# Optimization experiments

Measured on AMD Instinct MI355X. Metric: run time of the kernel, lower is better.

Reference implementation:

```python
import jax, jax.numpy as jnp
import numpy as np

EPS = 1e-10
BETA = 1.0  # beta passed to VectorQuantizer in Encoder_conv


def _conv(x, w, b, stride, pad):
    # x: NCHW, w: OIHW
    y = jax.lax.conv_general_dilated(x, w, window_strides=stride, padding=pad,
                                     dimension_numbers=('NCHW', 'OIHW', 'NCHW'))
    if b is not None:
        y = y + b[None, :, None, None]
    return y


def _forward(x, w_in, b_in, w_h1, b_h1, w_h2, b_h2, w_h3, b_h3,
             r0_w1, r0_w2, r1_w1, r1_w2, emb):
    relu = jax.nn.relu
    h = relu(_conv(x, w_in, b_in, (2, 2), [(1, 1), (1, 1)]))      # [B,128,256,256]
    h = relu(_conv(h, w_h1, b_h1, (4, 4), [(2, 2), (2, 2)]))      # [B,256,64,64]
    h = relu(_conv(h, w_h2, b_h2, (4, 4), [(2, 2), (2, 2)]))      # [B,256,16,16]
    h = relu(_conv(h, w_h3, b_h3, (2, 2), [(1, 1), (1, 1)]))      # [B,256,8,8]
    # ResidualBlock with 2 Residual layers: relu->conv[1,3]->relu->conv[1,1], no bias
    for wa, wb in ((r0_w1, r0_w2), (r1_w1, r1_w2)):
        t = _conv(relu(h), wa, None, (1, 1), [(0, 0), (1, 1)])
        t = _conv(relu(t), wb, None, (1, 1), [(0, 0), (0, 0)])
        h = h + t
    h = relu(h)
    # VectorQuantizer
    lat = jnp.transpose(h, (0, 2, 3, 1))                          # [B,H,W,D]
    D = emb.shape[1]
    flat = lat.reshape(-1, D)                                     # [N,D]
    dist = (jnp.sum(flat * flat, axis=1, keepdims=True)
            + jnp.sum(emb * emb, axis=1)
            - 2.0 * flat @ emb.T)                                 # [N,K]
    idx = jnp.argmin(dist, axis=1)                                # [N]
    quant = emb[idx].reshape(lat.shape)                           # [B,H,W,D]
    sg = jax.lax.stop_gradient
    e_loss = jnp.mean((sg(quant) - lat) ** 2)
    q_loss = jnp.mean((quant - sg(lat)) ** 2)
    loss = q_loss + BETA * e_loss
    quant_st = lat + sg(quant - lat)                              # straight-through
    probs = jnp.mean(jax.nn.one_hot(idx, emb.shape[0], dtype=lat.dtype), axis=0)
    perplexity = jnp.exp(-jnp.sum(probs * jnp.log(probs + EPS)))
    return jnp.transpose(quant_st, (0, 3, 1, 2)), loss, perplexity


def setup_inputs() -> dict:
    key = jax.random.key(0)
    ks = jax.random.split(key, 14)
    C_in, C, K = 3, 256, 512
    s = 0.05
    f32 = jnp.float32
    return {
        'x':     jax.random.normal(ks[0], (8, C_in, 512, 512), f32),
        'w_in':  jax.random.normal(ks[1], (C // 2, C_in, 4, 4), f32) * s,
        'b_in':  jnp.zeros((C // 2,), f32),
        'w_h1':  jax.random.normal(ks[2], (C, C // 2, 7, 7), f32) * s,
        'b_h1':  jnp.zeros((C,), f32),
        'w_h2':  jax.random.normal(ks[3], (C, C, 7, 7), f32) * s,
        'b_h2':  jnp.zeros((C,), f32),
        'w_h3':  jax.random.normal(ks[4], (C, C, 3, 3), f32) * s,
        'b_h3':  jnp.zeros((C,), f32),
        'r0_w1': jax.random.normal(ks[5], (4 * C, C, 1, 3), f32) * s,
        'r0_w2': jax.random.normal(ks[6], (C, 4 * C, 1, 1), f32) * s,
        'r1_w1': jax.random.normal(ks[7], (4 * C, C, 1, 3), f32) * s,
        'r1_w2': jax.random.normal(ks[8], (C, 4 * C, 1, 1), f32) * s,
        'emb':   jax.random.uniform(ks[9], (K, C), f32, -1.0 / K, 1.0 / K),
    }


def reference(x, w_in, b_in, w_h1, b_h1, w_h2, b_h2, w_h3, b_h3,
              r0_w1, r0_w2, r1_w1, r1_w2, emb):
    return _forward(x, w_in, b_in, w_h1, b_h1, w_h2, b_h2, w_h3, b_h3,
                    r0_w1, r0_w2, r1_w1, r1_w2, emb)
```

## Files before the change

### kernel.cpp

```cpp
#include <hip/hip_runtime.h>
#include <hip/hip_bf16.h>

typedef __hip_bfloat16 bf16;
typedef __attribute__((ext_vector_type(4))) float f32x4;
typedef __attribute__((ext_vector_type(8))) short short8;

__device__ __forceinline__ float b2f(bf16 v) { return __bfloat162float(v); }
__device__ __forceinline__ float bu2f(ushort u)
{
    union { uint i; float f; } c; c.i = (uint)u << 16; return c.f;
}
__device__ __forceinline__ ushort f2bu(float v)
{
    bf16 b = __float2bfloat16(v);
    return *(ushort*)&b;
}
__device__ __forceinline__ uint relu2(uint v)
{
    uint r = v;
    if (r & 0x8000u)     r &= 0xFFFF0000u;
    if (r & 0x80000000u) r &= 0x0000FFFFu;
    return r;
}
__device__ __forceinline__ uint packbf2(float a, float b)
{
    uint lo = f2bu(a), hi = f2bu(b);
    return lo | (hi << 16);
}

typedef const __attribute__((address_space(1))) unsigned int* as1_u32;
typedef __attribute__((address_space(3))) unsigned int* as3_u32;
__device__ __forceinline__ void gld16(const void* g, uint* l)
{
    __builtin_amdgcn_global_load_lds((as1_u32)g, (as3_u32)l, 16, 0, 0);
}

__global__ void init_k(const float* __restrict__ w_in, const float* __restrict__ w_h1,
        const float* __restrict__ w_h2, const float* __restrict__ w_h3,
        const float* __restrict__ r0w1, const float* __restrict__ r0w2,
        const float* __restrict__ r1w1, const float* __restrict__ r1w2,
        const float* __restrict__ emb,
        bf16* __restrict__ wp1, bf16* __restrict__ wpack2, bf16* __restrict__ wpack3,
        bf16* __restrict__ wp4, bf16* __restrict__ wpA0, bf16* __restrict__ wpA1,
        bf16* __restrict__ wpB0, bf16* __restrict__ wpB1,
        float* __restrict__ en, float* __restrict__ mse, int* __restrict__ hist,
        float* __restrict__ zpad, float* __restrict__ p3)
{
    long long i = (long long)blockIdx.x * 256 + threadIdx.x;
    if (i < 8192) {
        int j = i & 7; int co = (i >> 3) & 127; int kb = i >> 10;
        int k = kb * 8 + j;
        wp1[i] = __float2bfloat16(k < 48 ? w_in[co * 48 + k] : 0.f);
        return;
    }
    i -= 8192;
    if (i < 1638400) {
        int cil = i & 7; int co = (i >> 3) & 255; int r = i >> 11;
        int cib8 = r % 16; int tap = r / 16;
        float v = (tap < 49) ? w_h1[(size_t)co * 6272 + (cib8 * 8 + cil) * 49 + tap] : 0.f;
        wpack2[i] = __float2bfloat16(v);
        return;
    }
    i -= 1638400;
    if (i < 3276800) {
        int cil = i & 7; int co = (i >> 3) & 255; int r = i >> 11;
        int cib8 = r % 32; int tap = r / 32;
        float v = (tap < 49) ? w_h2[(size_t)co * 12544 + (cib8 * 8 + cil) * 49 + tap] : 0.f;
        wpack3[i] = __float2bfloat16(v);
        return;
    }
    i -= 3276800;
    if (i < 589824) {
        int cil = i & 7; int co = (i >> 3) & 255; int r = i >> 11;
        int cib8 = r % 32; int tap = r / 32;
        wp4[i] = __float2bfloat16(w_h3[(size_t)co * 2304 + (cib8 * 8 + cil) * 9 + tap]);
        return;
    }
    i -= 589824;
    if (i < 786432) {
        int cil = i & 7; int co = (i >> 3) & 1023; int r = i >> 13;
        int cib8 = r % 32; int tap = r / 32;
        wpA0[i] = __float2bfloat16(r0w1[(size_t)co * 768 + (cib8 * 8 + cil) * 3 + tap]);
        return;
    }
    i -= 786432;
    if (i < 786432) {
        int cil = i & 7; int co = (i >> 3) & 1023; int r = i >> 13;
        int cib8 = r % 32; int tap = r / 32;
        wpA1[i] = __float2bfloat16(r1w1[(size_t)co * 768 + (cib8 * 8 + cil) * 3 + tap]);
        return;
    }
    i -= 786432;
    if (i < 262144) {
        int cil = i & 7; int co = (i >> 3) & 255; int cib8 = (i >> 11) % 128;
        wpB0[i] = __float2bfloat16(r0w2[(size_t)co * 1024 + cib8 * 8 + cil]);
        return;
    }
    i -= 262144;
    if (i < 262144) {
        int cil = i & 7; int co = (i >> 3) & 255; int cib8 = (i >> 11) % 128;
        wpB1[i] = __float2bfloat16(r1w2[(size_t)co * 1024 + cib8 * 8 + cil]);
        return;
    }
    i -= 262144;
    if (i < 512) {
        const float* e = emb + (size_t)i * 256;
        float s = 0.f;
        for (int d = 0; d < 256; ++d) { float v = e[d]; s += v * v; }
        en[i] = s;
        return;
    }
    i -= 512;
    if (i < 577) {
        if (i == 0) mse[0] = 0.f;
        else if (i < 513) hist[i - 1] = 0;
        else zpad[i - 513] = 0.f;
        return;
    }
    i -= 577;
    if (i < 524288) p3[i] = 0.f;
}

__global__ __launch_bounds__(256) void conv1m_k(const float* __restrict__ x,
        const bf16* __restrict__ wp1, const float* __restrict__ bias,
        bf16* __restrict__ h1c)
{
    int bid = blockIdx.x;
    int pxt = bid & 511, img = bid >> 9;
    int tr = pxt >> 4, tc = pxt & 15;
    int oh0 = tr * 8, ow0 = tc * 16;
    const float* xi = x + (size_t)img * 786432;
    bf16* oT = h1c + (size_t)img * 8388608;

    int t = threadIdx.x;
    int wave = t >> 6, lane = t & 63;
    int quad = lane >> 4, l15 = lane & 15;

    __shared__ ushort xs[4 * 640];
    __shared__ ushort ot[128 * 136];

    int ihb = oh0 * 2 - 1, iwb = ow0 * 2 - 1;
    for (int i = t; i < 1836; i += 256) {
        int ci = i / 612; int r1 = i - ci * 612;
        int ihl = r1 / 34, iwl = r1 - ihl * 34;
        int ih = ihb + ihl, iw = iwb + iwl;
        float v = 0.f;
        if ((unsigned)ih < 512u && (unsigned)iw < 512u)
            v = xi[ci * 262144 + ih * 512 + iw];
        xs[ci * 640 + ihl * 35 + iwl] = f2bu(v);
    }
    for (int i = t; i < 640; i += 256) xs[3 * 640 + i] = 0;
    __syncthreads();

    f32x4 zero = {0.f, 0.f, 0.f, 0.f};
    f32x4 acc[8][2];
    #pragma unroll
    for (int m = 0; m < 8; ++m) { acc[m][0] = zero; acc[m][1] = zero; }

    int ci_b = quad >> 1;
    int kh0 = (quad & 1) * 2;
    int iwl0 = 2 * l15;

    #pragma unroll
    for (int ks = 0; ks < 2; ++ks) {
        union { short8 v; uint u[4]; } b[2];
        #pragma unroll
        for (int nt = 0; nt < 2; ++nt) {
            int py = wave * 2 + nt;
            int base = (ks * 2 + ci_b) * 640 + (2 * py + kh0) * 35 + iwl0;
            b[nt].u[0] = *(const uint*)&xs[base];
            b[nt].u[1] = *(const uint*)&xs[base + 2];
            b[nt].u[2] = *(const uint*)&xs[base + 35];
            b[nt].u[3] = *(const uint*)&xs[base + 37];
        }
        const bf16* abase = wp1 + ((size_t)(ks * 4 + quad) * 128 + l15) * 8;
        #pragma unroll
        for (int m = 0; m < 8; ++m) {
            short8 a = *(const short8*)(abase + m * 16 * 8);
            acc[m][0] = __builtin_amdgcn_mfma_f32_16x16x32_bf16(a, b[0].v, acc[m][0], 0, 0, 0);
            acc[m][1] = __builtin_amdgcn_mfma_f32_16x16x32_bf16(a, b[1].v, acc[m][1], 0, 0, 0);
        }
    }

    #pragma unroll
    for (int m = 0; m < 8; ++m) {
        int cobase = m * 16 + quad * 4;
        float b0 = bias[cobase], b1 = bias[cobase + 1];
        float b2 = bias[cobase + 2], b3 = bias[cobase + 3];
        #pragma unroll
        for (int nt = 0; nt < 2; ++nt) {
            int pxl = (wave * 2 + nt) * 16 + l15;
            uint w0 = packbf2(fmaxf(b0 + acc[m][nt][0], 0.f),
                              fmaxf(b1 + acc[m][nt][1], 0.f));
            uint w1 = packbf2(fmaxf(b2 + acc[m][nt][2], 0.f),
                              fmaxf(b3 + acc[m][nt][3], 0.f));
            *(uint*)&ot[pxl * 136 + cobase]     = w0;
            *(uint*)&ot[pxl * 136 + cobase + 2] = w1;
        }
    }
    __syncthreads();
    {
        int pxl = t >> 1, half = t & 1;
        int oh = oh0 + (pxl >> 4), ow = ow0 + (pxl & 15);
        size_t px = (size_t)(oh * 256 + ow);
        #pragma unroll
        for (int cb = 0; cb < 4; ++cb) {
            int c16 = half * 4 + cb;
            const uint4* src = (const uint4*)&ot[pxl * 136 + c16 * 16];
            uint4* dst = (uint4*)(oT + ((size_t)c16 * 65536 + px) * 16);
            dst[0] = src[0];
            dst[1] = src[1];
        }
    }
}

template <int IH, int OH, int CI, int SPLIT, int MODE>
__global__ __launch_bounds__(256) void conv_mfma6_k(
        const bf16* __restrict__ inC, const bf16* __restrict__ wpack,
        const float* __restrict__ bias, float* __restrict__ outA,
        bf16* __restrict__ outT, const float* __restrict__ zpad)
{
    constexpr int TPD = OH / 8;
    constexpr int NT = TPD * TPD;
    constexpr int CPB = (CI / 16) / SPLIT;
    constexpr int CIB8 = CI / 8;
    constexpr int NPX = IH * IH;
    constexpr int SLOTS = 2496;

    int bid = blockIdx.x;
    int pxt = bid % NT;
    int rest = bid / NT;
    int img = rest & 7;
    int split = rest >> 3;
    int oh0 = (pxt / TPD) * 8, ow0 = (pxt % TPD) * 8;

    int t = threadIdx.x;
    int wave = t >> 6, lane = t & 63;
    int quad = lane >> 4, l15 = lane & 15;

    const bf16* inb = inC + (size_t)img * ((size_t)NPX * CI);

    __shared__ __align__(16) uint bufA[SLOTS * 4];
    __shared__ __align__(16) uint bufB[SLOTS * 4];

    f32x4 zero = {0.f, 0.f, 0.f, 0.f};
    f32x4 acc[4][4];
    #pragma unroll
    for (int a = 0; a < 4; ++a)
        #pragma unroll
        for (int b = 0; b < 4; ++b) acc[a][b] = zero;

    int ihb = oh0 * 4 - 2, iwb = ow0 * 4 - 2;
    int qxl = l15 & 7, pyl = l15 >> 3;
    int tap_par = quad >> 1, ci_half = quad & 1;

    auto stage = [&](int ch, uint* dst) {
        const bf16* cb = inb + (size_t)ch * NPX * 16;
        auto issue = [&](int sb) {
            int p  = sb + lane;
            int pb = p << 4;
            int lb = pb ^ (((pb >> 7) & 7) << 4);
            int j  = lb >> 4;
            int pos = j >> 1, half = j & 1;
            int r = pos / 35, c = pos - r * 35;
            int ih = ihb + r, iw = iwb + c;
            const void* src = (const void*)zpad;
            if (j < 2450 && (unsigned)ih < (unsigned)IH && (unsigned)iw < (unsigned)IH)
                src = (const void*)(cb + ((size_t)ih * IH + iw) * 16 + half * 8);
            gld16(src, dst + sb * 4);
        };
        #pragma unroll
        for (int it = 0; it < 9; ++it) issue(it * 256 + wave * 64);
        if (wave < 3) issue(2304 + wave * 64);
    };

    auto compute = [&](int ch, const uint* cbuf) {
        const bf16* abase = wpack +
            ((size_t)(ch * 2 + ci_half) * 256 + wave * 64 + l15) * 8;
        for (int tp = 0; tp < 25; ++tp) {
            int tap = 2 * tp + tap_par;
            short8 a[4];
            #pragma unroll
            for (int ct = 0; ct < 4; ++ct)
                a[ct] = *(const short8*)(abase +
                    ((size_t)tap * CIB8 * 256 + ct * 16) * 8);
            int tapc = min(tap, 48);
            int kh = tapc / 7, kw = tapc - kh * 7;
            int p0 = (kh + 4 * pyl) * 35 + qxl * 4 + kw;
            #pragma unroll
            for (int pt = 0; pt < 4; ++pt) {
                int lb = ((p0 + pt * 280) * 2 + ci_half) << 4;
                int pb = lb ^ (((lb >> 7) & 7) << 4);
                short8 b = *(const short8*)((const char*)cbuf + pb);
                #pragma unroll
                for (int ct = 0; ct < 4; ++ct)
                    acc[ct][pt] = __builtin_amdgcn_mfma_f32_16x16x32_bf16(
                        a[ct], b, acc[ct][pt], 0, 0, 0);
            }
        }
    };

    stage(split * CPB, bufA);
    __syncthreads();
    for (int cc2 = 0; cc2 < CPB; cc2 += 2) {
        stage(split * CPB + cc2 + 1, bufB);
        compute(split * CPB + cc2, bufA);
        __syncthreads();
        if (cc2 + 2 < CPB) stage(split * CPB + cc2 + 2, bufA);
        compute(split * CPB + cc2 + 1, bufB);
        __syncthreads();
    }

    #pragma unroll
    for (int ct = 0; ct < 4; ++ct) {
        int cobase = wave * 64 + ct * 16 + quad * 4;
        #pragma unroll
        for (int pt = 0; pt < 4; ++pt) {
            int px = pt * 16 + l15;
            int oh = oh0 + (px >> 3), ow = ow0 + (px & 7);
            int pxg = oh * OH + ow;
            #pragma unroll
            for (int r = 0; r < 4; ++r) {
                int co = cobase + r;
                float v = acc[ct][pt][r];
                if (MODE == 1) {
                    atomicAdd(&outA[(size_t)img * (OH * OH * 256)
                                    + (size_t)co * (OH * OH) + pxg], v);
                } else {
                    float o = (MODE == 0) ? fmaxf(bias[co] + v, 0.f) : v;
                    size_t base = (size_t)((MODE == 2 ? split * 8 : 0) + img)
                                  * (size_t)(OH * OH * 256);
                    outT[base + ((size_t)(co >> 4) * (OH * OH) + pxg) * 16 + (co & 15)]
                        = __float2bfloat16(o);
                }
            }
        }
    }
}

__global__ void combine2_k(const bf16* __restrict__ p2s, const float* __restrict__ bias,
                           bf16* __restrict__ h2c)
{
    int i4 = blockIdx.x * 256 + threadIdx.x;
    int idx = i4 << 2;
    const ushort* ps = (const ushort*)p2s;
    ushort4 s0 = *(const ushort4*)(ps + idx);
    ushort4 s1 = *(const ushort4*)(ps + 8388608 + idx);
    int rem = idx & 1048575;
    int co0 = ((rem >> 16) << 4) | (idx & 15);
    ushort4 o;
    o.x = f2bu(fmaxf(bias[co0 + 0] + bu2f(s0.x) + bu2f(s1.x), 0.f));
    o.y = f2bu(fmaxf(bias[co0 + 1] + bu2f(s0.y) + bu2f(s1.y), 0.f));
    o.z = f2bu(fmaxf(bias[co0 + 2] + bu2f(s0.z) + bu2f(s1.z), 0.f));
    o.w = f2bu(fmaxf(bias[co0 + 3] + bu2f(s0.w) + bu2f(s1.w), 0.f));
    *(ushort4*)((ushort*)h2c + idx) = o;
}

__global__ void combine3_k(const float* __restrict__ p3, const float* __restrict__ bias,
                           bf16* __restrict__ h3T)
{
    int idx = blockIdx.x * 256 + threadIdx.x;
    int px = idx & 255;
    int co = (idx >> 8) & 255;
    int img = idx >> 16;
    float v = fmaxf(bias[co] + p3[idx], 0.f);
    h3T[((size_t)img * 256 + px) * 256 + co] = __float2bfloat16(v);
}

__global__ __launch_bounds__(256) void conv4m_k(const bf16* __restrict__ h3T,
        const bf16* __restrict__ wp4, const float* __restrict__ bias,
        bf16* __restrict__ h4T)
{
    int bid = blockIdx.x;
    int img = bid >> 2, cog = bid & 3;
    int t = threadIdx.x;
    int wave = t >> 6, lane = t & 63;
    int quad = lane >> 4, l15 = lane & 15;

    __shared__ uint pt[16 * 325];

    for (int i = t; i < 16 * 325; i += 256) pt[i] = 0;

    f32x4 zero = {0.f, 0.f, 0.f, 0.f};
    f32x4 acc[4];
    #pragma unroll
    for (int b = 0; b < 4; ++b) acc[b] = zero;

    const bf16* inb = h3T + (size_t)img * 65536;

    for (int ch = 0; ch < 8; ++ch) {
        __syncthreads();
        for (int e = t; e < 4096; e += 256) {
            int cp = e & 15, px = e >> 4;
            int py = px >> 4, qx = px & 15;
            uint v = *(const uint*)(inb + (size_t)px * 256 + ch * 32 + cp * 2);
            pt[cp * 325 + (py + 1) * 18 + qx + 1] = v;
        }
        __syncthreads();

        for (int tap = 0; tap < 9; ++tap) {
            int kh = tap / 3, kw = tap - kh * 3;
            const bf16* abase = wp4 + ((size_t)((tap * 32 + ch * 4 + quad) * 256)
                                       + cog * 64 + wave * 16 + l15) * 8;
            short8 a = *(const short8*)abase;
            #pragma unroll
            for (int pq = 0; pq < 4; ++pq) {
                int pyo = 2 * pq + (l15 >> 3);
                int ipos = (2 * pyo + kh) * 18 + 2 * (l15 & 7) + kw;
                union { short8 v; uint u[4]; } b;
                b.u[0] = pt[(quad * 4 + 0) * 325 + ipos];
                b.u[1] = pt[(quad * 4 + 1) * 325 + ipos];
                b.u[2] = pt[(quad * 4 + 2) * 325 + ipos];
                b.u[3] = pt[(quad * 4 + 3) * 325 + ipos];
                acc[pq] = __builtin_amdgcn_mfma_f32_16x16x32_bf16(
                    a, b.v, acc[pq], 0, 0, 0);
            }
        }
    }

    int cobase = cog * 64 + wave * 16 + quad * 4;
    #pragma unroll
    for (int pq = 0; pq < 4; ++pq) {
        int px = pq * 16 + l15;
        #pragma unroll
        for (int r = 0; r < 4; ++r) {
            int co = cobase + r;
            float v = fmaxf(bias[co] + acc[pq][r], 0.f);
            h4T[((size_t)img * 64 + px) * 256 + co] = __float2bfloat16(v);
        }
    }
}

__global__ __launch_bounds__(256) void resam_k(const bf16* __restrict__ hT,
        const bf16* __restrict__ wpA, bf16* __restrict__ t1T)
{
    int bid = blockIdx.x;
    int img = bid >> 3, g = bid & 7;
    int t = threadIdx.x;
    int wave = t >> 6, lane = t & 63;
    int quad = lane >> 4, l15 = lane & 15;

    __shared__ uint ph[128 * 81];

    for (int i = t; i < 128 * 81; i += 256) ph[i] = 0;
    __syncthreads();
    const bf16* inb = hT + (size_t)img * 16384;
    for (int e = t; e < 8192; e += 256) {
        int cp = e & 127, px = e >> 7;
        uint v = relu2(*(const uint*)(inb + (size_t)px * 256 + cp * 2));
        ph[cp * 81 + (px >> 3) * 10 + (px & 7) + 1] = v;
    }
    __syncthreads();

    f32x4 zero = {0.f, 0.f, 0.f, 0.f};
    f32x4 acc[2][4];
    #pragma unroll
    for (int a = 0; a < 2; ++a)
        #pragma unroll
        for (int b = 0; b < 4; ++b) acc[a][b] = zero;

    for (int ch = 0; ch < 8; ++ch) {
        for (int tap = 0; tap < 3; ++tap) {
            const bf16* abase = wpA + ((size_t)(tap * 32 + ch * 4 + quad) * 1024
                                       + g * 128 + wave * 32 + l15) * 8;
            short8 a[2];
            #pragma unroll
            for (int ct = 0; ct < 2; ++ct)
                a[ct] = *(const short8*)(abase + ct * 16 * 8);
            #pragma unroll
            for (int pq = 0; pq < 4; ++pq) {
                int py = 2 * pq + (l15 >> 3);
                int pos = py * 10 + (l15 & 7) + tap;
                union { short8 v; uint u[4]; } b;
                b.u[0] = ph[(ch * 16 + quad * 4 + 0) * 81 + pos];
                b.u[1] = ph[(ch * 16 + quad * 4 + 1) * 81 + pos];
                b.u[2] = ph[(ch * 16 + quad * 4 + 2) * 81 + pos];
                b.u[3] = ph[(ch * 16 + quad * 4 + 3) * 81 + pos];
                #pragma unroll
                for (int ct = 0; ct < 2; ++ct)
                    acc[ct][pq] = __builtin_amdgcn_mfma_f32_16x16x32_bf16(
                        a[ct], b.v, acc[ct][pq], 0, 0, 0);
            }
        }
    }

    #pragma unroll
    for (int ct = 0; ct < 2; ++ct) {
        int cobase = g * 128 + wave * 32 + ct * 16 + quad * 4;
        #pragma unroll
        for (int pq = 0; pq < 4; ++pq) {
            int px = pq * 16 + l15;
            #pragma unroll
            for (int r = 0; r < 4; ++r)
                t1T[((size_t)img * 64 + px) * 1024 + cobase + r]
                    = __float2bfloat16(acc[ct][pq][r]);
        }
    }
}

__global__ __launch_bounds__(256) void resbm_k(const bf16* __restrict__ holdT,
        const bf16* __restrict__ t1T, const bf16* __restrict__ wpB,
        bf16* __restrict__ hnewT)
{
    int bid = blockIdx.x;
    int img = bid >> 2, cog = bid & 3;
    int t = threadIdx.x;
    int wave = t >> 6, lane = t & 63;
    int quad = lane >> 4, l15 = lane & 15;

    __shared__ uint pb[256 * 65];

    f32x4 zero = {0.f, 0.f, 0.f, 0.f};
    f32x4 acc[4];
    #pragma unroll
    for (int b = 0; b < 4; ++b) acc[b] = zero;

    const bf16* inb = t1T + (size_t)img * 65536;

    for (int s = 0; s < 2; ++s) {
        __syncthreads();
        for (int e = t; e < 16384; e += 256) {
            int cp = e & 255, px = e >> 8;
            uint v = relu2(*(const uint*)(inb + (size_t)px * 1024 + s * 512 + cp * 2));
            pb[cp * 65 + px] = v;
        }
        __syncthreads();

        for (int chl = 0; chl < 16; ++chl) {
            int ch = s * 16 + chl;
            const bf16* abase = wpB + ((size_t)(ch * 4 + quad) * 256
                                       + cog * 64 + wave * 16 + l15) * 8;
            short8 a = *(const short8*)abase;
            #pragma unroll
            for (int pq = 0; pq < 4; ++pq) {
                int px = pq * 16 + l15;
                union { short8 v; uint u[4]; } b;
                b.u[0] = pb[(chl * 16 + quad * 4 + 0) * 65 + px];
                b.u[1] = pb[(chl * 16 + quad * 4 + 1) * 65 + px];
                b.u[2] = pb[(chl * 16 + quad * 4 + 2) * 65 + px];
                b.u[3] = pb[(chl * 16 + quad * 4 + 3) * 65 + px];
                acc[pq] = __builtin_amdgcn_mfma_f32_16x16x32_bf16(
                    a, b.v, acc[pq], 0, 0, 0);
            }
        }
    }

    int cobase = cog * 64 + wave * 16 + quad * 4;
    #pragma unroll
    for (int pq = 0; pq < 4; ++pq) {
        int px = pq * 16 + l15;
        #pragma unroll
        for (int r = 0; r < 4; ++r) {
            int co = cobase + r;
            size_t o = ((size_t)img * 64 + px) * 256 + co;
            float v = b2f(holdT[o]) + acc[pq][r];
            hnewT[o] = __float2bfloat16(v);
        }
    }
}

__global__ void vq_k(const bf16* __restrict__ h6T, const float* __restrict__ emb,
                     const float* __restrict__ en, float* __restrict__ out,
                     float* __restrict__ mse_acc, int* __restrict__ hist)
{
    int row = blockIdx.x;
    int b = row >> 6, y = (row >> 3) & 7, xx = row & 7;
    int t = threadIdx.x;
    __shared__ float lat[256];
    __shared__ float sdist[256];
    __shared__ int   sidx[256];

    float l = fmaxf(b2f(h6T[(size_t)row * 256 + t]), 0.f);
    lat[t] = l;
    __syncthreads();

    float d0 = 0.f, d1 = 0.f;
    const float* e0 = emb + (size_t)t * 256;
    const float* e1 = emb + (size_t)(t + 256) * 256;
    for (int d = 0; d < 256; ++d) {
        float lv = lat[d];
        d0 += lv * e0[d];
        d1 += lv * e1[d];
    }
    d0 = en[t] - 2.f * d0;
    d1 = en[t + 256] - 2.f * d1;
    float best_d = d0; int best_i = t;
    if (d1 < best_d) { best_d = d1; best_i = t + 256; }
    sdist[t] = best_d; sidx[t] = best_i;
    __syncthreads();
    for (int s = 128; s > 0; s >>= 1) {
        if (t < s) {
            float od = sdist[t + s]; int oi = sidx[t + s];
            if (od < sdist[t] || (od == sdist[t] && oi < sidx[t])) {
                sdist[t] = od; sidx[t] = oi;
            }
        }
        __syncthreads();
    }
    int idx = sidx[0];

    float q = emb[(size_t)idx * 256 + t];
    out[((size_t)(b * 256 + t) * 8 + y) * 8 + xx] = q;
    float diff = q - lat[t];
    __syncthreads();
    sdist[t] = diff * diff;
    __syncthreads();
    for (int s = 128; s > 0; s >>= 1) {
        if (t < s) sdist[t] += sdist[t + s];
        __syncthreads();
    }
    if (t == 0) {
        atomicAdd(mse_acc, sdist[0]);
        atomicAdd(&hist[idx], 1);
    }
}

__global__ void final_k(const float* __restrict__ mse_acc, const int* __restrict__ hist,
                        float* __restrict__ out)
{
    __shared__ float sh[512];
    int t = threadIdx.x;
    float p = (float)hist[t] / 512.f;
    sh[t] = p * logf(p + 1e-10f);
    __syncthreads();
    for (int s = 256; s > 0; s >>= 1) {
        if (t < s) sh[t] += sh[t + s];
        __syncthreads();
    }
    if (t == 0) {
        float loss = 2.f * mse_acc[0] / (512.f * 256.f);
        float perp = expf(-sh[0]);
        out[131072] = loss;
        out[131073] = perp;
    }
}

extern "C" void kernel_launch(void* const* d_in, const int* in_sizes, int n_in,
                              void* d_out, int out_size, void* d_ws, size_t ws_size,
                              hipStream_t stream)
{
    const float* x    = (const float*)d_in[0];
    const float* w_in = (const float*)d_in[1];
    const float* b_in = (const float*)d_in[2];
    const float* w_h1 = (const float*)d_in[3];
    const float* b_h1 = (const float*)d_in[4];
    const float* w_h2 = (const float*)d_in[5];
    const float* b_h2 = (const float*)d_in[6];
    const float* w_h3 = (const float*)d_in[7];
    const float* b_h3 = (const float*)d_in[8];
    const float* r0w1 = (const float*)d_in[9];
    const float* r0w2 = (const float*)d_in[10];
    const float* r1w1 = (const float*)d_in[11];
    const float* r1w2 = (const float*)d_in[12];
    const float* emb  = (const float*)d_in[13];
    float* out = (float*)d_out;

    char* ws = (char*)d_ws;
    size_t off = 0;
    auto alloc = [&](size_t bytes) -> void* {
        void* p = ws + off;
        off += (bytes + 255) & ~(size_t)255;
        return p;
    };

    float* en  = (float*)alloc(512 * 4);
    float* mse = (float*)alloc(256);
    int*  hist = (int*)alloc(512 * 4);
    float* zpad = (float*)alloc(256);
    float* p3  = (float*)alloc(524288ull * 4);
    bf16* h3T  = (bf16*)alloc(524288ull * 2);
    bf16* h4T  = (bf16*)alloc(131072ull * 2);
    bf16* t1T  = (bf16*)alloc(524288ull * 2);
    bf16* h5T  = (bf16*)alloc(131072ull * 2);
    bf16* h6T  = (bf16*)alloc(131072ull * 2);
    bf16* wp1  = (bf16*)alloc(8192ull * 2);
    bf16* wpack2 = (bf16*)alloc(1638400ull * 2);
    bf16* wpack3 = (bf16*)alloc(3276800ull * 2);
    bf16* wp4  = (bf16*)alloc(589824ull * 2);
    bf16* wpA0 = (bf16*)alloc(786432ull * 2);
    bf16* wpA1 = (bf16*)alloc(786432ull * 2);
    bf16* wpB0 = (bf16*)alloc(262144ull * 2);
    bf16* wpB1 = (bf16*)alloc(262144ull * 2);
    bf16* h2c  = (bf16*)alloc(8388608ull * 2);
    size_t base_end = off;

    const size_t P2S_B = 16777216ull * 2;
    const size_t H1F_B = 8388608ull * 8 * 2;
    size_t needT0 = base_end + P2S_B + H1F_B + 4096;
    size_t needT1 = base_end + H1F_B + 4096;
    bf16* p2s = nullptr;
    bf16* h1c;
    int tier;
    if (ws_size >= needT0) {
        p2s = (bf16*)alloc(P2S_B);
        h1c = (bf16*)alloc(H1F_B);
        tier = 0;
    } else if (ws_size >= needT1) {
        h1c = (bf16*)alloc(H1F_B);
        tier = 1;
    } else {
        h1c = (bf16*)alloc(8388608ull * 2);
        tier = 2;
    }

    init_k<<<31781, 256, 0, stream>>>(w_in, w_h1, w_h2, w_h3, r0w1, r0w2, r1w1, r1w2,
        emb, wp1, wpack2, wpack3, wp4, wpA0, wpA1, wpB0, wpB1, en, mse, hist, zpad, p3);

    if (tier == 0) {
        conv1m_k<<<4096, 256, 0, stream>>>(x, wp1, b_in, h1c);
        conv_mfma6_k<256, 64, 128, 2, 2><<<1024, 256, 0, stream>>>(
            h1c, wpack2, nullptr, nullptr, p2s, zpad);
        combine2_k<<<8192, 256, 0, stream>>>(p2s, b_h1, h2c);
    } else if (tier == 1) {
        conv1m_k<<<4096, 256, 0, stream>>>(x, wp1, b_in, h1c);
        conv_mfma6_k<256, 64, 128, 1, 0><<<512, 256, 0, stream>>>(
            h1c, wpack2, b_h1, nullptr, h2c, zpad);
    } else {
        for (int n = 0; n < 8; ++n) {
            conv1m_k<<<512, 256, 0, stream>>>(x + (size_t)n * 786432, wp1, b_in, h1c);
            conv_mfma6_k<256, 64, 128, 1, 0><<<64, 256, 0, stream>>>(
                h1c, wpack2, b_h1, nullptr, h2c + (size_t)n * 1048576, zpad);
        }
    }

    conv_mfma6_k<64, 16, 256, 8, 1><<<256, 256, 0, stream>>>(
        h2c, wpack3, b_h2, p3, nullptr, zpad);
    combine3_k<<<2048, 256, 0, stream>>>(p3, b_h2, h3T);

    conv4m_k<<<32, 256, 0, stream>>>(h3T, wp4, b_h3, h4T);
    resam_k<<<64, 256, 0, stream>>>(h4T, wpA0, t1T);
    resbm_k<<<32, 256, 0, stream>>>(h4T, t1T, wpB0, h5T);
    resam_k<<<64, 256, 0, stream>>>(h5T, wpA1, t1T);
    resbm_k<<<32, 256, 0, stream>>>(h5T, t1T, wpB1, h6T);

    vq_k<<<512, 256, 0, stream>>>(h6T, emb, en, out, mse, hist);
    final_k<<<1, 512, 0, stream>>>(mse, hist, out);
}
```

Baseline: 511.2 us.

## Rework conv MFMA staging, split-K partials, drop combine2, batch VQ rows

Several changes land together. The main conv kernel now precomputes staging addresses once, fully unrolls the tap loop with constant LDS offsets, raises wave priority around the MFMA section and requests two blocks per CU. The split-channel conv3 path writes per-split partial buffers that combine3 sums, replacing float atomics and the zeroing of p3. The split-K tier for conv2 and its combine kernel are removed. The VQ kernel handles four rows per block with wave-shuffle reductions. These cut address arithmetic, atomic contention and launch count, at the cost of more register pressure, 8x more partial-buffer traffic, and fewer blocks for the conv2 stage when the big workspace is available.

Result: faster. 466.3 us (-8.8%).

```diff
diff --git a/kernel.cpp b/kernel.cpp
--- a/kernel.cpp
+++ b/kernel.cpp
@@ -6,10 +6,6 @@
 typedef __attribute__((ext_vector_type(8))) short short8;
 
 __device__ __forceinline__ float b2f(bf16 v) { return __bfloat162float(v); }
-__device__ __forceinline__ float bu2f(ushort u)
-{
-    union { uint i; float f; } c; c.i = (uint)u << 16; return c.f;
-}
 __device__ __forceinline__ ushort f2bu(float v)
 {
     bf16 b = __float2bfloat16(v);
@@ -44,7 +40,7 @@
         bf16* __restrict__ wp4, bf16* __restrict__ wpA0, bf16* __restrict__ wpA1,
         bf16* __restrict__ wpB0, bf16* __restrict__ wpB1,
         float* __restrict__ en, float* __restrict__ mse, int* __restrict__ hist,
-        float* __restrict__ zpad, float* __restrict__ p3)
+        float* __restrict__ zpad)
 {
     long long i = (long long)blockIdx.x * 256 + threadIdx.x;
     if (i < 8192) {
@@ -115,10 +111,7 @@
         if (i == 0) mse[0] = 0.f;
         else if (i < 513) hist[i - 1] = 0;
         else zpad[i - 513] = 0.f;
-        return;
-    }
-    i -= 577;
-    if (i < 524288) p3[i] = 0.f;
+    }
 }
 
 __global__ __launch_bounds__(256) void conv1m_k(const float* __restrict__ x,
@@ -215,7 +208,7 @@
 }
 
 template <int IH, int OH, int CI, int SPLIT, int MODE>
-__global__ __launch_bounds__(256) void conv_mfma6_k(
+__global__ __launch_bounds__(256, 2) void conv_mfma7_k(
         const bf16* __restrict__ inC, const bf16* __restrict__ wpack,
         const float* __restrict__ bias, float* __restrict__ outA,
         bf16* __restrict__ outT, const float* __restrict__ zpad)
@@ -254,50 +247,67 @@
     int qxl = l15 & 7, pyl = l15 >> 3;
     int tap_par = quad >> 1, ci_half = quad & 1;
 
+    int  srel[10];
+    bool sval[10];
+    #pragma unroll
+    for (int it = 0; it < 10; ++it) {
+        int sb = (it < 9) ? it * 256 + wave * 64 : 2304 + wave * 64;
+        int p  = sb + lane;
+        int pb = p << 4;
+        int lb = pb ^ (((pb >> 7) & 7) << 4);
+        int j  = lb >> 4;
+        int pos = j >> 1, half = j & 1;
+        int r = pos / 35, c = pos - r * 35;
+        int ih = ihb + r, iw = iwb + c;
+        sval[it] = (j < 2450) && ((unsigned)ih < (unsigned)IH)
+                   && ((unsigned)iw < (unsigned)IH);
+        srel[it] = (ih * IH + iw) * 16 + half * 8;
+    }
+
     auto stage = [&](int ch, uint* dst) {
-        const bf16* cb = inb + (size_t)ch * NPX * 16;
-        auto issue = [&](int sb) {
-            int p  = sb + lane;
-            int pb = p << 4;
-            int lb = pb ^ (((pb >> 7) & 7) << 4);
-            int j  = lb >> 4;
-            int pos = j >> 1, half = j & 1;
-            int r = pos / 35, c = pos - r * 35;
-            int ih = ihb + r, iw = iwb + c;
-            const void* src = (const void*)zpad;
-            if (j < 2450 && (unsigned)ih < (unsigned)IH && (unsigned)iw < (unsigned)IH)
-                src = (const void*)(cb + ((size_t)ih * IH + iw) * 16 + half * 8);
+        const bf16* cbp = inb + (size_t)ch * NPX * 16;
+        #pragma unroll
+        for (int it = 0; it < 10; ++it) {
+            if (it == 9 && wave >= 3) continue;
+            int sb = (it < 9) ? it * 256 + wave * 64 : 2304 + wave * 64;
+            const void* src = sval[it] ? (const void*)(cbp + srel[it])
+                                       : (const void*)zpad;
             gld16(src, dst + sb * 4);
-        };
-        #pragma unroll
-        for (int it = 0; it < 9; ++it) issue(it * 256 + wave * 64);
-        if (wave < 3) issue(2304 + wave * 64);
+        }
     };
 
+    int rbase = pyl * 4480 + qxl * 128 + ci_half * 16;
+    int d1  = tap_par * 32;
+    int d29 = tap_par * 928;
+
     auto compute = [&](int ch, const uint* cbuf) {
-        const bf16* abase = wpack +
-            ((size_t)(ch * 2 + ci_half) * 256 + wave * 64 + l15) * 8;
+        const bf16* ab = wpack
+            + ((size_t)(ch * 2 + ci_half) * 256 + wave * 64 + l15) * 8
+            + (size_t)tap_par * (CIB8 * 2048);
+        __builtin_amdgcn_s_setprio(1);
+        #pragma unroll
         for (int tp = 0; tp < 25; ++tp) {
-            int tap = 2 * tp + tap_par;
-            short8 a[4];
-            #pragma unroll
-            for (int ct = 0; ct < 4; ++ct)
-                a[ct] = *(const short8*)(abase +
-                    ((size_t)tap * CIB8 * 256 + ct * 16) * 8);
-            int tapc = min(tap, 48);
-            int kh = tapc / 7, kw = tapc - kh * 7;
-            int p0 = (kh + 4 * pyl) * 35 + qxl * 4 + kw;
+            const int kh0 = (2 * tp) / 7, kw0 = (2 * tp) % 7;
+            const int cE  = (kh0 * 35 + kw0) * 32;
+            int dsel = (tp == 24) ? 0 : ((kw0 == 6) ? d29 : d1);
+            int lbb  = rbase + cE + dsel;
+            const bf16* at = ab + (size_t)(2 * tp) * (CIB8 * 2048);
+            short8 a0 = *(const short8*)(at);
+            short8 a1 = *(const short8*)(at + 128);
+            short8 a2 = *(const short8*)(at + 256);
+            short8 a3 = *(const short8*)(at + 384);
             #pragma unroll
             for (int pt = 0; pt < 4; ++pt) {
-                int lb = ((p0 + pt * 280) * 2 + ci_half) << 4;
+                int lb = lbb + pt * 8960;
                 int pb = lb ^ (((lb >> 7) & 7) << 4);
                 short8 b = *(const short8*)((const char*)cbuf + pb);
-                #pragma unroll
-                for (int ct = 0; ct < 4; ++ct)
-                    acc[ct][pt] = __builtin_amdgcn_mfma_f32_16x16x32_bf16(
-                        a[ct], b, acc[ct][pt], 0, 0, 0);
+                acc[0][pt] = __builtin_amdgcn_mfma_f32_16x16x32_bf16(a0, b, acc[0][pt], 0, 0, 0);
+                acc[1][pt] = __builtin_amdgcn_mfma_f32_16x16x32_bf16(a1, b, acc[1][pt], 0, 0, 0);
+                acc[2][pt] = __builtin_amdgcn_mfma_f32_16x16x32_bf16(a2, b, acc[2][pt], 0, 0, 0);
+                acc[3][pt] = __builtin_amdgcn_mfma_f32_16x16x32_bf16(a3, b, acc[3][pt], 0, 0, 0);
             }
         }
+        __builtin_amdgcn_s_setprio(0);
     };
 
     stage(split * CPB, bufA);
@@ -323,13 +333,13 @@
             for (int r = 0; r < 4; ++r) {
                 int co = cobase + r;
                 float v = acc[ct][pt][r];
-                if (MODE == 1) {
-                    atomicAdd(&outA[(size_t)img * (OH * OH * 256)
-                                    + (size_t)co * (OH * OH) + pxg], v);
+                if (MODE == 3) {
+                    outA[(size_t)split * ((size_t)8 * OH * OH * 256)
+                         + (size_t)img * (OH * OH * 256)
+                         + (size_t)co * (OH * OH) + pxg] = v;
                 } else {
-                    float o = (MODE == 0) ? fmaxf(bias[co] + v, 0.f) : v;
-                    size_t base = (size_t)((MODE == 2 ? split * 8 : 0) + img)
-                                  * (size_t)(OH * OH * 256);
+                    float o = fmaxf(bias[co] + v, 0.f);
+                    size_t base = (size_t)img * (size_t)(OH * OH * 256);
                     outT[base + ((size_t)(co >> 4) * (OH * OH) + pxg) * 16 + (co & 15)]
                         = __float2bfloat16(o);
                 }
@@ -338,24 +348,6 @@
     }
 }
 
-__global__ void combine2_k(const bf16* __restrict__ p2s, const float* __restrict__ bias,
-                           bf16* __restrict__ h2c)
-{
-    int i4 = blockIdx.x * 256 + threadIdx.x;
-    int idx = i4 << 2;
-    const ushort* ps = (const ushort*)p2s;
-    ushort4 s0 = *(const ushort4*)(ps + idx);
-    ushort4 s1 = *(const ushort4*)(ps + 8388608 + idx);
-    int rem = idx & 1048575;
-    int co0 = ((rem >> 16) << 4) | (idx & 15);
-    ushort4 o;
-    o.x = f2bu(fmaxf(bias[co0 + 0] + bu2f(s0.x) + bu2f(s1.x), 0.f));
-    o.y = f2bu(fmaxf(bias[co0 + 1] + bu2f(s0.y) + bu2f(s1.y), 0.f));
-    o.z = f2bu(fmaxf(bias[co0 + 2] + bu2f(s0.z) + bu2f(s1.z), 0.f));
-    o.w = f2bu(fmaxf(bias[co0 + 3] + bu2f(s0.w) + bu2f(s1.w), 0.f));
-    *(ushort4*)((ushort*)h2c + idx) = o;
-}
-
 __global__ void combine3_k(const float* __restrict__ p3, const float* __restrict__ bias,
                            bf16* __restrict__ h3T)
 {
@@ -363,7 +355,10 @@
     int px = idx & 255;
     int co = (idx >> 8) & 255;
     int img = idx >> 16;
-    float v = fmaxf(bias[co] + p3[idx], 0.f);
+    float v = bias[co];
+    #pragma unroll
+    for (int s = 0; s < 8; ++s) v += p3[(size_t)s * 524288 + idx];
+    v = fmaxf(v, 0.f);
     h3T[((size_t)img * 256 + px) * 256 + co] = __float2bfloat16(v);
 }
 
@@ -559,60 +554,86 @@
     }
 }
 
-__global__ void vq_k(const bf16* __restrict__ h6T, const float* __restrict__ emb,
-                     const float* __restrict__ en, float* __restrict__ out,
-                     float* __restrict__ mse_acc, int* __restrict__ hist)
-{
-    int row = blockIdx.x;
-    int b = row >> 6, y = (row >> 3) & 7, xx = row & 7;
+__global__ __launch_bounds__(256) void vq_k(const bf16* __restrict__ h6T,
+        const float* __restrict__ emb, const float* __restrict__ en,
+        float* __restrict__ out, float* __restrict__ mse_acc, int* __restrict__ hist)
+{
+    int row0 = blockIdx.x * 4;
     int t = threadIdx.x;
-    __shared__ float lat[256];
-    __shared__ float sdist[256];
-    __shared__ int   sidx[256];
-
-    float l = fmaxf(b2f(h6T[(size_t)row * 256 + t]), 0.f);
-    lat[t] = l;
-    __syncthreads();
-
-    float d0 = 0.f, d1 = 0.f;
-    const float* e0 = emb + (size_t)t * 256;
-    const float* e1 = emb + (size_t)(t + 256) * 256;
-    for (int d = 0; d < 256; ++d) {
-        float lv = lat[d];
-        d0 += lv * e0[d];
-        d1 += lv * e1[d];
-    }
-    d0 = en[t] - 2.f * d0;
-    d1 = en[t + 256] - 2.f * d1;
-    float best_d = d0; int best_i = t;
-    if (d1 < best_d) { best_d = d1; best_i = t + 256; }
-    sdist[t] = best_d; sidx[t] = best_i;
-    __syncthreads();
-    for (int s = 128; s > 0; s >>= 1) {
-        if (t < s) {
-            float od = sdist[t + s]; int oi = sidx[t + s];
-            if (od < sdist[t] || (od == sdist[t] && oi < sidx[t])) {
-                sdist[t] = od; sidx[t] = oi;
-            }
-        }
-        __syncthreads();
-    }
-    int idx = sidx[0];
-
-    float q = emb[(size_t)idx * 256 + t];
-    out[((size_t)(b * 256 + t) * 8 + y) * 8 + xx] = q;
-    float diff = q - lat[t];
-    __syncthreads();
-    sdist[t] = diff * diff;
-    __syncthreads();
-    for (int s = 128; s > 0; s >>= 1) {
-        if (t < s) sdist[t] += sdist[t + s];
-        __syncthreads();
-    }
-    if (t == 0) {
-        atomicAdd(mse_acc, sdist[0]);
-        atomicAdd(&hist[idx], 1);
-    }
+    int wave = t >> 6, lane = t & 63;
+    __shared__ float lat[4][256];
+    __shared__ float swd[4][4];
+    __shared__ int   swi[4][4];
+    __shared__ int   fidx[4];
+    __shared__ float smse[4];
+
+    for (int e = t; e < 1024; e += 256) {
+        int r = e >> 8, c = e & 255;
+        lat[r][c] = fmaxf(b2f(h6T[(size_t)(row0 + r) * 256 + c]), 0.f);
+    }
+    __syncthreads();
+
+    float a0[4] = {0.f, 0.f, 0.f, 0.f}, a1[4] = {0.f, 0.f, 0.f, 0.f};
+    const float4* e0 = (const float4*)(emb + (size_t)t * 256);
+    const float4* e1 = (const float4*)(emb + (size_t)(t + 256) * 256);
+    for (int d4 = 0; d4 < 64; ++d4) {
+        float4 v0 = e0[d4], v1 = e1[d4];
+        #pragma unroll
+        for (int r = 0; r < 4; ++r) {
+            float l0 = lat[r][d4 * 4], l1 = lat[r][d4 * 4 + 1];
+            float l2 = lat[r][d4 * 4 + 2], l3 = lat[r][d4 * 4 + 3];
+            a0[r] += l0 * v0.x + l1 * v0.y + l2 * v0.z + l3 * v0.w;
+            a1[r] += l0 * v1.x + l1 * v1.y + l2 * v1.z + l3 * v1.w;
+        }
+    }
+    float en0 = en[t], en1 = en[t + 256];
+    float bd[4]; int bi[4];
+    #pragma unroll
+    for (int r = 0; r < 4; ++r) {
+        float d0 = en0 - 2.f * a0[r], d1v = en1 - 2.f * a1[r];
+        bd[r] = d0; bi[r] = t;
+        if (d1v < bd[r]) { bd[r] = d1v; bi[r] = t + 256; }
+    }
+    #pragma unroll
+    for (int s = 1; s < 64; s <<= 1) {
+        #pragma unroll
+        for (int r = 0; r < 4; ++r) {
+            float od = __shfl_xor(bd[r], s);
+            int   oi = __shfl_xor(bi[r], s);
+            if (od < bd[r] || (od == bd[r] && oi < bi[r])) { bd[r] = od; bi[r] = oi; }
+        }
+    }
+    if (lane == 0) {
+        #pragma unroll
+        for (int r = 0; r < 4; ++r) { swd[wave][r] = bd[r]; swi[wave][r] = bi[r]; }
+    }
+    __syncthreads();
+    if (t < 4) {
+        float best = swd[0][t]; int bidx = swi[0][t];
+        for (int w = 1; w < 4; ++w) {
+            float od = swd[w][t]; int oi = swi[w][t];
+            if (od < best || (od == best && oi < bidx)) { best = od; bidx = oi; }
+        }
+        fidx[t] = bidx;
+    }
+    __syncthreads();
+
+    float msel = 0.f;
+    #pragma unroll
+    for (int r = 0; r < 4; ++r) {
+        int row = row0 + r;
+        int b = row >> 6, y = (row >> 3) & 7, xx = row & 7;
+        float q = emb[(size_t)fidx[r] * 256 + t];
+        out[((size_t)(b * 256 + t) * 8 + y) * 8 + xx] = q;
+        float diff = q - lat[r][t];
+        msel += diff * diff;
+    }
+    #pragma unroll
+    for (int s = 1; s < 64; s <<= 1) msel += __shfl_xor(msel, s);
+    if (lane == 0) smse[wave] = msel;
+    __syncthreads();
+    if (t == 0) atomicAdd(mse_acc, smse[0] + smse[1] + smse[2] + smse[3]);
+    if (t < 4) atomicAdd(&hist[fidx[t]], 1);
 }
 
 __global__ void final_k(const float* __restrict__ mse_acc, const int* __restrict__ hist,
@@ -667,7 +688,7 @@
     float* mse = (float*)alloc(256);
     int*  hist = (int*)alloc(512 * 4);
     float* zpad = (float*)alloc(256);
-    float* p3  = (float*)alloc(524288ull * 4);
+    float* p3  = (float*)alloc(4194304ull * 4);
     bf16* h3T  = (bf16*)alloc(524288ull * 2);
     bf16* h4T  = (bf16*)alloc(131072ull * 2);
     bf16* t1T  = (bf16*)alloc(524288ull * 2);
@@ -684,18 +705,11 @@
     bf16* h2c  = (bf16*)alloc(8388608ull * 2);
     size_t base_end = off;
 
-    const size_t P2S_B = 16777216ull * 2;
     const size_t H1F_B = 8388608ull * 8 * 2;
-    size_t needT0 = base_end + P2S_B + H1F_B + 4096;
     size_t needT1 = base_end + H1F_B + 4096;
-    bf16* p2s = nullptr;
     bf16* h1c;
     int tier;
-    if (ws_size >= needT0) {
-        p2s = (bf16*)alloc(P2S_B);
-        h1c = (bf16*)alloc(H1F_B);
-        tier = 0;
-    } else if (ws_size >= needT1) {
+    if (ws_size >= needT1) {
         h1c = (bf16*)alloc(H1F_B);
         tier = 1;
     } else {
@@ -703,28 +717,23 @@
         tier = 2;
     }
 
-    init_k<<<31781, 256, 0, stream>>>(w_in, w_h1, w_h2, w_h3, r0w1, r0w2, r1w1, r1w2,
-        emb, wp1, wpack2, wpack3, wp4, wpA0, wpA1, wpB0, wpB1, en, mse, hist, zpad, p3);
-
-    if (tier == 0) {
+    init_k<<<29733, 256, 0, stream>>>(w_in, w_h1, w_h2, w_h3, r0w1, r0w2, r1w1, r1w2,
+        emb, wp1, wpack2, wpack3, wp4, wpA0, wpA1, wpB0, wpB1, en, mse, hist, zpad);
+
+    if (tier == 1) {
         conv1m_k<<<4096, 256, 0, stream>>>(x, wp1, b_in, h1c);
-        conv_mfma6_k<256, 64, 128, 2, 2><<<1024, 256, 0, stream>>>(
-            h1c, wpack2, nullptr, nullptr, p2s, zpad);
-        combine2_k<<<8192, 256, 0, stream>>>(p2s, b_h1, h2c);
-    } else if (tier == 1) {
-        conv1m_k<<<4096, 256, 0, stream>>>(x, wp1, b_in, h1c);
-        conv_mfma6_k<256, 64, 128, 1, 0><<<512, 256, 0, stream>>>(
+        conv_mfma7_k<256, 64, 128, 1, 0><<<512, 256, 0, stream>>>(
             h1c, wpack2, b_h1, nullptr, h2c, zpad);
     } else {
         for (int n = 0; n < 8; ++n) {
             conv1m_k<<<512, 256, 0, stream>>>(x + (size_t)n * 786432, wp1, b_in, h1c);
-            conv_mfma6_k<256, 64, 128, 1, 0><<<64, 256, 0, stream>>>(
+            conv_mfma7_k<256, 64, 128, 1, 0><<<64, 256, 0, stream>>>(
                 h1c, wpack2, b_h1, nullptr, h2c + (size_t)n * 1048576, zpad);
         }
     }
 
-    conv_mfma6_k<64, 16, 256, 8, 1><<<256, 256, 0, stream>>>(
-        h2c, wpack3, b_h2, p3, nullptr, zpad);
+    conv_mfma7_k<64, 16, 256, 8, 3><<<256, 256, 0, stream>>>(
+        h2c, wpack3, nullptr, p3, nullptr, zpad);
     combine3_k<<<2048, 256, 0, stream>>>(p3, b_h2, h3T);
 
     conv4m_k<<<32, 256, 0, stream>>>(h3T, wp4, b_h3, h4T);
@@ -733,6 +742,6 @@
     resam_k<<<64, 256, 0, stream>>>(h5T, wpA1, t1T);
     resbm_k<<<32, 256, 0, stream>>>(h5T, t1T, wpB1, h6T);
 
-    vq_k<<<512, 256, 0, stream>>>(h6T, emb, en, out, mse, hist);
+    vq_k<<<128, 256, 0, stream>>>(h6T, emb, en, out, mse, hist);
     final_k<<<1, 512, 0, stream>>>(mse, hist, out);
 }
```
